# Kernel optimization log

Measured on AMD Instinct MI355X. Metric: run time of the kernel, lower is better.

## Reference

```python
import jax, jax.numpy as jnp
import numpy as np
from jax import lax

EMB, H1, H2 = 100, 128, 64  # embedding_dim, hidden_dim, hidden_dim//2
B, T = 1024, 512


def _uniform(key, shape, scale):
    return jax.random.uniform(key, shape, jnp.float32, -scale, scale)


def setup_inputs() -> dict:
    key = jax.random.key(0)
    ks = jax.random.split(key, 16)
    s1 = 1.0 / np.sqrt(H1)
    s2 = 1.0 / np.sqrt(H2)
    return {
        "X": jax.random.normal(ks[0], (B, T, EMB), jnp.float32),
        # PyTorch LSTM weights, gate order (i, f, g, o)
        "W1_ih": _uniform(ks[1], (4 * H1, EMB), s1),
        "W1_hh": _uniform(ks[2], (4 * H1, H1), s1),
        "b1_ih": _uniform(ks[3], (4 * H1,), s1),
        "b1_hh": _uniform(ks[4], (4 * H1,), s1),
        "W2_ih": _uniform(ks[5], (4 * H2, H1), s2),
        "W2_hh": _uniform(ks[6], (4 * H2, H2), s2),
        "b2_ih": _uniform(ks[7], (4 * H2,), s2),
        "b2_hh": _uniform(ks[8], (4 * H2,), s2),
        "fc1_w": _uniform(ks[9], (32, H2), 1.0 / np.sqrt(H2)),
        "fc1_b": _uniform(ks[10], (32,), 1.0 / np.sqrt(H2)),
        "fc2_w": _uniform(ks[11], (1, 32), 1.0 / np.sqrt(32)),
        "fc2_b": _uniform(ks[12], (1,), 1.0 / np.sqrt(32)),
    }


def _lstm(x, W_ih, W_hh, b_ih, b_hh):
    # x: [B, T, D]; returns (all hidden states [B, T, H], final h [B, H])
    Bb = x.shape[0]
    H = W_hh.shape[1]
    # Batch the input projection across all timesteps (one big GEMM).
    xw = jnp.einsum('btd,gd->tbg', x, W_ih) + (b_ih + b_hh)  # [T, B, 4H]

    def step(carry, xt):
        h, c = carry
        gates = xt + h @ W_hh.T  # [B, 4H]
        i, f, g, o = jnp.split(gates, 4, axis=-1)
        c = jax.nn.sigmoid(f) * c + jax.nn.sigmoid(i) * jnp.tanh(g)
        h = jax.nn.sigmoid(o) * jnp.tanh(c)
        return (h, c), h

    h0 = jnp.zeros((Bb, H), x.dtype)
    (h_n, _), hs = lax.scan(step, (h0, h0), xw)
    return jnp.swapaxes(hs, 0, 1), h_n


def reference(X, W1_ih, W1_hh, b1_ih, b1_hh,
              W2_ih, W2_hh, b2_ih, b2_hh,
              fc1_w, fc1_b, fc2_w, fc2_b):
    hs1, _ = _lstm(X, W1_ih, W1_hh, b1_ih, b1_hh)        # [B, T, 128]
    # dropout is identity at inference
    _, h_n = _lstm(hs1, W2_ih, W2_hh, b2_ih, b2_hh)      # [B, 64]
    x = jax.nn.relu(h_n @ fc1_w.T + fc1_b)               # [B, 32]
    x = x @ fc2_w.T + fc2_b                              # [B, 1]
    return jax.nn.sigmoid(x)[:, 0]                       # [B]
```

## Files before the change

### kernel.cpp

```cpp
#include <hip/hip_runtime.h>
#include <hip/hip_fp16.h>

typedef _Float16 half8 __attribute__((ext_vector_type(8)));
typedef _Float16 half4 __attribute__((ext_vector_type(4)));
typedef float floatx4 __attribute__((ext_vector_type(4)));

#define TT 512
#define EE 100
#define NBATCH 16
#define NBLK 64
#define WS_NEED ((size_t)NBLK * TT * 2048 * sizeof(_Float16))

typedef const __attribute__((address_space(1))) void gvoid_t;
typedef __attribute__((address_space(3))) void lvoid_t;

#define MFMA16 __builtin_amdgcn_mfma_f32_16x16x32_f16

__device__ __forceinline__ float sigm(float x) {
    return __builtin_amdgcn_rcpf(1.0f + __expf(-x));
}
__device__ __forceinline__ float tanh_(float x) {
    return __builtin_amdgcn_rcpf(1.0f + __expf(-2.0f * x)) * 2.0f - 1.0f;
}
__device__ __forceinline__ half4 cvt4(float4 v) {
    half4 h; h[0] = (_Float16)v.x; h[1] = (_Float16)v.y; h[2] = (_Float16)v.z; h[3] = (_Float16)v.w;
    return h;
}

extern "C" __global__ void __launch_bounds__(256)
xfrag_prep(const float* __restrict__ X, _Float16* __restrict__ xw)
{
    const int g   = blockIdx.x >> 5;
    const int t0  = (blockIdx.x & 31) << 4;
    const int tid = threadIdx.x;

    __shared__ __align__(16) _Float16 tile[16][16][120];

    for (int mm = 0; mm < 16; ++mm) {
        const float4* src = (const float4*)(X + ((size_t)(g * 16 + mm) * TT + t0) * EE);
#pragma unroll
        for (int r = 0; r < 2; ++r) {
            const int idx = tid + r * 256;
            if (idx < 400) {
                float4 v = src[idx];
                const int tt = idx / 25, kk = idx - 25 * tt;
                *(half4*)&tile[tt][mm][4 * kk] = cvt4(v);
            }
        }
    }
    __syncthreads();

    const int c = tid >> 4, mm = tid & 15;
    for (int tt = 0; tt < 16; ++tt) {
        half8 v;
        if (c < 12) {
            v = *(const half8*)&tile[tt][mm][8 * c];
        } else if (c == 12) {
            half4 lo = *(const half4*)&tile[tt][mm][96];
            v[0] = lo[0]; v[1] = lo[1]; v[2] = lo[2]; v[3] = lo[3];
            v[4] = (_Float16)1.0f;
            v[5] = (_Float16)0.0f; v[6] = (_Float16)0.0f; v[7] = (_Float16)0.0f;
        } else {
#pragma unroll
            for (int j = 0; j < 8; ++j) v[j] = (_Float16)0.0f;
        }
        *(half8*)&xw[((size_t)(g * TT) + t0 + tt) * 2048 + c * 128 + mm * 8] = v;
    }
}

template<int USE_WS>
__global__ void __launch_bounds__(512, 1)
lstm_regc(const float* __restrict__ X, const _Float16* __restrict__ xw,
          const float* __restrict__ W1ih, const float* __restrict__ W1hh,
          const float* __restrict__ b1i,  const float* __restrict__ b1h,
          const float* __restrict__ W2ih, const float* __restrict__ W2hh,
          const float* __restrict__ b2i,  const float* __restrict__ b2h,
          const float* __restrict__ fc1w, const float* __restrict__ fc1b,
          const float* __restrict__ fc2w, const float* __restrict__ fc2b,
          float* __restrict__ out)
{
    const int tid  = threadIdx.x;
    const int w    = tid >> 6;
    const int lane = tid & 63;
    const int q    = lane >> 4;
    const int m    = lane & 15;
    const int b0   = blockIdx.x * NBATCH;

    __shared__ __align__(16) _Float16 h1b[2 * 2048];
    __shared__ __align__(16) _Float16 h2b[2 * 1024];
    __shared__ __align__(16) _Float16 xb [2 * 2048];
    __shared__ float fca[NBATCH][32];

    for (int i = tid; i < 2 * 1024; i += 512) h2b[i] = (_Float16)0.0f;
    if (!USE_WS) {
        for (int i = tid; i < 2 * 2048; i += 512) {
            const int k = i & 2047;
            xb[i] = (k >= 1536 && k < 1664 && (k & 7) == 4) ? (_Float16)1.0f
                                                            : (_Float16)0.0f;
        }
    }

    half8 w1ihf[4][4], w1hhf[4][4], w2ihf[2][4], w2hhf[2][2];
    floatx4 bias2v[2];
#pragma unroll
    for (int g = 0; g < 4; ++g) {
        const int r = g * 128 + 16 * w + m;
        const float bias = b1i[r] + b1h[r];
#pragma unroll
        for (int s = 0; s < 4; ++s) {
            half8 f;
#pragma unroll
            for (int j = 0; j < 8; ++j) {
                const int k = 32 * s + 8 * q + j;
                float v = 0.0f;
                if (k < EE) v = W1ih[r * EE + k];
                else if (k == EE) v = bias;
                f[j] = (_Float16)v;
            }
            w1ihf[g][s] = f;
        }
#pragma unroll
        for (int s = 0; s < 4; ++s) {
            half8 f;
#pragma unroll
            for (int j = 0; j < 8; ++j) f[j] = (_Float16)W1hh[r * 128 + 32 * s + 8 * q + j];
            w1hhf[g][s] = f;
        }
    }
#pragma unroll
    for (int tau = 0; tau < 2; ++tau) {
        const int rr = (m & 3) * 64 + 8 * w + 4 * tau + (m >> 2);
#pragma unroll
        for (int s = 0; s < 4; ++s) {
            half8 f;
#pragma unroll
            for (int j = 0; j < 8; ++j) f[j] = (_Float16)W2ih[rr * 128 + 32 * s + 8 * q + j];
            w2ihf[tau][s] = f;
        }
#pragma unroll
        for (int s = 0; s < 2; ++s) {
            half8 f;
#pragma unroll
            for (int j = 0; j < 8; ++j) f[j] = (_Float16)W2hh[rr * 64 + 32 * s + 8 * q + j];
            w2hhf[tau][s] = f;
        }
        const int uu = 8 * w + 4 * tau + q;
#pragma unroll
        for (int reg = 0; reg < 4; ++reg)
            bias2v[tau][reg] = b2i[reg * 64 + uu] + b2h[reg * 64 + uu];
    }

    const int foff  = q * 128 + m * 8;
    const int vv    = 2 * w + (q >> 1);
    const int jj    = 4 * (q & 1);
    const int woff1 = (vv >> 2) * 512 + (vv & 3) * 128 + m * 8 + jj;
    int uoff[2];
#pragma unroll
    for (int tau = 0; tau < 2; ++tau) {
        const int u = 8 * w + 4 * tau + q;
        uoff[tau] = (u >> 5) * 512 + ((u >> 3) & 3) * 128 + m * 8 + (u & 7);
    }

    const _Float16* xwb = xw + (size_t)blockIdx.x * TT * 2048;

    int gaddr = 0, laddr = 0;
    bool xval = false;
    float4 xr = {0.f, 0.f, 0.f, 0.f};
    if (!USE_WS) {
        xval = tid < 400;
        const int f = xval ? tid : 0;
        const int n = f / 25, pp = f - 25 * n, e0 = 4 * pp;
        gaddr = (b0 + n) * (TT * EE) + e0;
        const int s = e0 >> 5, qr = (e0 >> 3) & 3, j0 = e0 & 7;
        laddr = ((s * 4 + qr) * 16 + n) * 8 + j0;
    }

    __syncthreads();

    if (USE_WS) {
        if (w < 4) {
            __builtin_amdgcn_global_load_lds((gvoid_t*)(xwb + 0 * 2048 + w * 512 + lane * 8),
                                             (lvoid_t*)(xb + 0 * 2048 + w * 512), 16, 0, 0);
            __builtin_amdgcn_global_load_lds((gvoid_t*)(xwb + 1 * 2048 + w * 512 + lane * 8),
                                             (lvoid_t*)(xb + 1 * 2048 + w * 512), 16, 0, 0);
        }
    } else if (xval) {
        *(half4*)&xb[0 * 2048 + laddr] = cvt4(*(const float4*)&X[gaddr + 0 * EE]);
        *(half4*)&xb[1 * 2048 + laddr] = cvt4(*(const float4*)&X[gaddr + 1 * EE]);
        xr = *(const float4*)&X[gaddr + 2 * EE];
    }
    __syncthreads();

    half8 bx[4], bh[4];
#pragma unroll
    for (int s = 0; s < 4; ++s) {
        bx[s] = *(const half8*)(xb + 0 * 2048 + s * 512 + foff);
#pragma unroll
        for (int j = 0; j < 8; ++j) bh[s][j] = (_Float16)0.0f;
    }

    floatx4 c1 = {0.f, 0.f, 0.f, 0.f};
    float c2[2] = {0.f, 0.f};

#pragma unroll 1
    for (int t = 0; t < TT; ++t) {
        const int cur = t & 1, nxt = cur ^ 1;

        {
            floatx4 a[4];
#pragma unroll
            for (int g = 0; g < 4; ++g) a[g] = (floatx4){0.f, 0.f, 0.f, 0.f};
#pragma unroll
            for (int s = 0; s < 4; ++s) {
#pragma unroll
                for (int g = 0; g < 4; ++g) a[g] = MFMA16(w1ihf[g][s], bx[s], a[g], 0, 0, 0);
            }
#pragma unroll
            for (int s = 0; s < 4; ++s) {
#pragma unroll
                for (int g = 0; g < 4; ++g) a[g] = MFMA16(w1hhf[g][s], bh[s], a[g], 0, 0, 0);
            }
            half4 hv;
#pragma unroll
            for (int r = 0; r < 4; ++r) {
                const float iv = sigm(a[0][r]);
                const float fv = sigm(a[1][r]);
                const float gv = tanh_(a[2][r]);
                const float ov = sigm(a[3][r]);
                const float c  = fv * c1[r] + iv * gv;
                c1[r] = c;
                hv[r] = (_Float16)(ov * tanh_(c));
            }
            *(half4*)&h1b[cur * 2048 + woff1] = hv;
        }
        __syncthreads();

        if (USE_WS) {
            if (w < 4) {
                const int tn = (t + 2 < TT) ? (t + 2) : (TT - 1);
                __builtin_amdgcn_global_load_lds((gvoid_t*)(xwb + (size_t)tn * 2048 + w * 512 + lane * 8),
                                                 (lvoid_t*)(xb + cur * 2048 + w * 512), 16, 0, 0);
            }
        } else if (xval) {
            *(half4*)&xb[cur * 2048 + laddr] = cvt4(xr);
            const int tn = (t + 3 < TT) ? (t + 3) : (TT - 1);
            xr = *(const float4*)&X[gaddr + tn * EE];
        }

        half8 h2f[2];
#pragma unroll
        for (int s = 0; s < 4; ++s) bh[s] = *(const half8*)(h1b + cur * 2048 + s * 512 + foff);
#pragma unroll
        for (int s = 0; s < 2; ++s) h2f[s] = *(const half8*)(h2b + nxt * 1024 + s * 512 + foff);
#pragma unroll
        for (int s = 0; s < 4; ++s) bx[s] = *(const half8*)(xb + nxt * 2048 + s * 512 + foff);

        floatx4 a2[2] = { bias2v[0], bias2v[1] };
#pragma unroll
        for (int s = 0; s < 4; ++s) {
            a2[0] = MFMA16(w2ihf[0][s], bh[s], a2[0], 0, 0, 0);
            a2[1] = MFMA16(w2ihf[1][s], bh[s], a2[1], 0, 0, 0);
        }
#pragma unroll
        for (int s = 0; s < 2; ++s) {
            a2[0] = MFMA16(w2hhf[0][s], h2f[s], a2[0], 0, 0, 0);
            a2[1] = MFMA16(w2hhf[1][s], h2f[s], a2[1], 0, 0, 0);
        }

#pragma unroll
        for (int tau = 0; tau < 2; ++tau) {
            const float iv = sigm(a2[tau][0]);
            const float fv = sigm(a2[tau][1]);
            const float gv = tanh_(a2[tau][2]);
            const float ov = sigm(a2[tau][3]);
            const float c  = fv * c2[tau] + iv * gv;
            c2[tau] = c;
            h2b[cur * 1024 + uoff[tau]] = (_Float16)(ov * tanh_(c));
        }
    }
    __syncthreads();

    {
        const int nb = tid >> 5, o = tid & 31;
        const _Float16* h2p = h2b + 1024 + nb * 8;
        float s = fc1b[o];
#pragma unroll
        for (int k = 0; k < 64; ++k)
            s += fc1w[o * 64 + k] * (float)h2p[(k >> 5) * 512 + ((k >> 3) & 3) * 128 + (k & 7)];
        fca[nb][o] = fmaxf(s, 0.0f);
    }
    __syncthreads();
    if (tid < NBATCH) {
        float s = fc2b[0];
#pragma unroll
        for (int k = 0; k < 32; ++k) s += fc2w[k] * fca[tid][k];
        out[b0 + tid] = sigm(s);
    }
}

extern "C" void kernel_launch(void* const* d_in, const int* in_sizes, int n_in,
                              void* d_out, int out_size, void* d_ws, size_t ws_size,
                              hipStream_t stream) {
    const float* X    = (const float*)d_in[0];
    const float* W1ih = (const float*)d_in[1];
    const float* W1hh = (const float*)d_in[2];
    const float* b1i  = (const float*)d_in[3];
    const float* b1h  = (const float*)d_in[4];
    const float* W2ih = (const float*)d_in[5];
    const float* W2hh = (const float*)d_in[6];
    const float* b2i  = (const float*)d_in[7];
    const float* b2h  = (const float*)d_in[8];
    const float* fc1w = (const float*)d_in[9];
    const float* fc1b = (const float*)d_in[10];
    const float* fc2w = (const float*)d_in[11];
    const float* fc2b = (const float*)d_in[12];
    _Float16* xw = (_Float16*)d_ws;

    if (ws_size >= WS_NEED) {
        hipLaunchKernelGGL(xfrag_prep, dim3(2048), dim3(256), 0, stream, X, xw);
        hipLaunchKernelGGL(lstm_regc<1>, dim3(NBLK), dim3(512), 0, stream,
                           X, xw, W1ih, W1hh, b1i, b1h, W2ih, W2hh, b2i, b2h,
                           fc1w, fc1b, fc2w, fc2b, (float*)d_out);
    } else {
        hipLaunchKernelGGL(lstm_regc<0>, dim3(NBLK), dim3(512), 0, stream,
                           X, xw, W1ih, W1hh, b1i, b1h, W2ih, W2hh, b2i, b2h,
                           fc1w, fc1b, fc2w, fc2b, (float*)d_out);
    }
}
```

Baseline: 1.129 ms.

## Fuse X conversion, software-pipeline the two LSTM layers in one barrier per step

Drops the separate X-to-fp16 prep kernel and workspace path. X is now loaded and converted inside the recurrent kernel through a triple-buffered LDS ring. The loop is restructured so layer 2 for step t-1 and layer 1 for step t run in the same iteration with a single barrier, interleaving their MFMAs and activations, plus a tail step for the last layer-2 update. Gate weights and biases are pre-scaled by -log2(e) or -2log2(e), so sigmoid and tanh use a raw exp2 plus rcp; this adds a little fp16 rounding of the scaled weights.

```diff
diff --git a/kernel.cpp b/kernel.cpp
--- a/kernel.cpp
+++ b/kernel.cpp
@@ -9,75 +9,31 @@
 #define EE 100
 #define NBATCH 16
 #define NBLK 64
-#define WS_NEED ((size_t)NBLK * TT * 2048 * sizeof(_Float16))
-
-typedef const __attribute__((address_space(1))) void gvoid_t;
-typedef __attribute__((address_space(3))) void lvoid_t;
 
 #define MFMA16 __builtin_amdgcn_mfma_f32_16x16x32_f16
-
-__device__ __forceinline__ float sigm(float x) {
-    return __builtin_amdgcn_rcpf(1.0f + __expf(-x));
-}
-__device__ __forceinline__ float tanh_(float x) {
-    return __builtin_amdgcn_rcpf(1.0f + __expf(-2.0f * x)) * 2.0f - 1.0f;
+#define EXP2   __builtin_amdgcn_exp2f
+#define RCP    __builtin_amdgcn_rcpf
+
+#define S_SIG  (-1.44269504088896340736f)
+#define S_TANH (-2.88539008177792681472f)
+
+__device__ __forceinline__ float sigm_slow(float x) {
+    return RCP(1.0f + __expf(-x));
 }
 __device__ __forceinline__ half4 cvt4(float4 v) {
     half4 h; h[0] = (_Float16)v.x; h[1] = (_Float16)v.y; h[2] = (_Float16)v.z; h[3] = (_Float16)v.w;
     return h;
 }
 
-extern "C" __global__ void __launch_bounds__(256)
-xfrag_prep(const float* __restrict__ X, _Float16* __restrict__ xw)
-{
-    const int g   = blockIdx.x >> 5;
-    const int t0  = (blockIdx.x & 31) << 4;
-    const int tid = threadIdx.x;
-
-    __shared__ __align__(16) _Float16 tile[16][16][120];
-
-    for (int mm = 0; mm < 16; ++mm) {
-        const float4* src = (const float4*)(X + ((size_t)(g * 16 + mm) * TT + t0) * EE);
-#pragma unroll
-        for (int r = 0; r < 2; ++r) {
-            const int idx = tid + r * 256;
-            if (idx < 400) {
-                float4 v = src[idx];
-                const int tt = idx / 25, kk = idx - 25 * tt;
-                *(half4*)&tile[tt][mm][4 * kk] = cvt4(v);
-            }
-        }
-    }
-    __syncthreads();
-
-    const int c = tid >> 4, mm = tid & 15;
-    for (int tt = 0; tt < 16; ++tt) {
-        half8 v;
-        if (c < 12) {
-            v = *(const half8*)&tile[tt][mm][8 * c];
-        } else if (c == 12) {
-            half4 lo = *(const half4*)&tile[tt][mm][96];
-            v[0] = lo[0]; v[1] = lo[1]; v[2] = lo[2]; v[3] = lo[3];
-            v[4] = (_Float16)1.0f;
-            v[5] = (_Float16)0.0f; v[6] = (_Float16)0.0f; v[7] = (_Float16)0.0f;
-        } else {
-#pragma unroll
-            for (int j = 0; j < 8; ++j) v[j] = (_Float16)0.0f;
-        }
-        *(half8*)&xw[((size_t)(g * TT) + t0 + tt) * 2048 + c * 128 + mm * 8] = v;
-    }
-}
-
-template<int USE_WS>
 __global__ void __launch_bounds__(512, 1)
-lstm_regc(const float* __restrict__ X, const _Float16* __restrict__ xw,
-          const float* __restrict__ W1ih, const float* __restrict__ W1hh,
-          const float* __restrict__ b1i,  const float* __restrict__ b1h,
-          const float* __restrict__ W2ih, const float* __restrict__ W2hh,
-          const float* __restrict__ b2i,  const float* __restrict__ b2h,
-          const float* __restrict__ fc1w, const float* __restrict__ fc1b,
-          const float* __restrict__ fc2w, const float* __restrict__ fc2b,
-          float* __restrict__ out)
+lstm_fused(const float* __restrict__ X,
+           const float* __restrict__ W1ih, const float* __restrict__ W1hh,
+           const float* __restrict__ b1i,  const float* __restrict__ b1h,
+           const float* __restrict__ W2ih, const float* __restrict__ W2hh,
+           const float* __restrict__ b2i,  const float* __restrict__ b2h,
+           const float* __restrict__ fc1w, const float* __restrict__ fc1b,
+           const float* __restrict__ fc2w, const float* __restrict__ fc2b,
+           float* __restrict__ out)
 {
     const int tid  = threadIdx.x;
     const int w    = tid >> 6;
@@ -88,24 +44,24 @@
 
     __shared__ __align__(16) _Float16 h1b[2 * 2048];
     __shared__ __align__(16) _Float16 h2b[2 * 1024];
-    __shared__ __align__(16) _Float16 xb [2 * 2048];
+    __shared__ __align__(16) _Float16 xb [3 * 2048];
     __shared__ float fca[NBATCH][32];
 
-    for (int i = tid; i < 2 * 1024; i += 512) h2b[i] = (_Float16)0.0f;
-    if (!USE_WS) {
-        for (int i = tid; i < 2 * 2048; i += 512) {
-            const int k = i & 2047;
-            xb[i] = (k >= 1536 && k < 1664 && (k & 7) == 4) ? (_Float16)1.0f
-                                                            : (_Float16)0.0f;
-        }
-    }
+    for (int i = tid; i < 3 * 2048; i += 512) {
+        const int k = i & 2047;
+        xb[i] = (k >= 1536 && k < 1664 && (k & 7) == 4) ? (_Float16)1.0f
+                                                        : (_Float16)0.0f;
+    }
+    for (int i = tid; i < 2048; i += 512) h1b[2048 + i] = (_Float16)0.0f;
+    for (int i = tid; i < 1024; i += 512) h2b[i] = (_Float16)0.0f;
 
     half8 w1ihf[4][4], w1hhf[4][4], w2ihf[2][4], w2hhf[2][2];
     floatx4 bias2v[2];
 #pragma unroll
     for (int g = 0; g < 4; ++g) {
+        const float sg = (g == 2) ? S_TANH : S_SIG;
         const int r = g * 128 + 16 * w + m;
-        const float bias = b1i[r] + b1h[r];
+        const float bias = (b1i[r] + b1h[r]) * sg;
 #pragma unroll
         for (int s = 0; s < 4; ++s) {
             half8 f;
@@ -113,7 +69,7 @@
             for (int j = 0; j < 8; ++j) {
                 const int k = 32 * s + 8 * q + j;
                 float v = 0.0f;
-                if (k < EE) v = W1ih[r * EE + k];
+                if (k < EE) v = W1ih[r * EE + k] * sg;
                 else if (k == EE) v = bias;
                 f[j] = (_Float16)v;
             }
@@ -123,31 +79,36 @@
         for (int s = 0; s < 4; ++s) {
             half8 f;
 #pragma unroll
-            for (int j = 0; j < 8; ++j) f[j] = (_Float16)W1hh[r * 128 + 32 * s + 8 * q + j];
+            for (int j = 0; j < 8; ++j)
+                f[j] = (_Float16)(W1hh[r * 128 + 32 * s + 8 * q + j] * sg);
             w1hhf[g][s] = f;
         }
     }
 #pragma unroll
     for (int tau = 0; tau < 2; ++tau) {
+        const float srow = ((m & 3) == 2) ? S_TANH : S_SIG;
         const int rr = (m & 3) * 64 + 8 * w + 4 * tau + (m >> 2);
 #pragma unroll
         for (int s = 0; s < 4; ++s) {
             half8 f;
 #pragma unroll
-            for (int j = 0; j < 8; ++j) f[j] = (_Float16)W2ih[rr * 128 + 32 * s + 8 * q + j];
+            for (int j = 0; j < 8; ++j)
+                f[j] = (_Float16)(W2ih[rr * 128 + 32 * s + 8 * q + j] * srow);
             w2ihf[tau][s] = f;
         }
 #pragma unroll
         for (int s = 0; s < 2; ++s) {
             half8 f;
 #pragma unroll
-            for (int j = 0; j < 8; ++j) f[j] = (_Float16)W2hh[rr * 64 + 32 * s + 8 * q + j];
+            for (int j = 0; j < 8; ++j)
+                f[j] = (_Float16)(W2hh[rr * 64 + 32 * s + 8 * q + j] * srow);
             w2hhf[tau][s] = f;
         }
         const int uu = 8 * w + 4 * tau + q;
 #pragma unroll
         for (int reg = 0; reg < 4; ++reg)
-            bias2v[tau][reg] = b2i[reg * 64 + uu] + b2h[reg * 64 + uu];
+            bias2v[tau][reg] = (b2i[reg * 64 + uu] + b2h[reg * 64 + uu])
+                               * ((reg == 2) ? S_TANH : S_SIG);
     }
 
     const int foff  = q * 128 + m * 8;
@@ -161,101 +122,48 @@
         uoff[tau] = (u >> 5) * 512 + ((u >> 3) & 3) * 128 + m * 8 + (u & 7);
     }
 
-    const _Float16* xwb = xw + (size_t)blockIdx.x * TT * 2048;
-
-    int gaddr = 0, laddr = 0;
-    bool xval = false;
+    const bool xval = tid < 400;
+    const int f    = xval ? tid : 0;
+    const int n    = f / 25, pp = f - 25 * n, e0 = 4 * pp;
+    const int gaddr = (b0 + n) * (TT * EE) + e0;
+    const int ls = e0 >> 5, lq = (e0 >> 3) & 3, lj = e0 & 7;
+    const int laddr = ls * 512 + lq * 128 + n * 8 + lj;
+
     float4 xr = {0.f, 0.f, 0.f, 0.f};
-    if (!USE_WS) {
-        xval = tid < 400;
-        const int f = xval ? tid : 0;
-        const int n = f / 25, pp = f - 25 * n, e0 = 4 * pp;
-        gaddr = (b0 + n) * (TT * EE) + e0;
-        const int s = e0 >> 5, qr = (e0 >> 3) & 3, j0 = e0 & 7;
-        laddr = ((s * 4 + qr) * 16 + n) * 8 + j0;
-    }
-
-    __syncthreads();
-
-    if (USE_WS) {
-        if (w < 4) {
-            __builtin_amdgcn_global_load_lds((gvoid_t*)(xwb + 0 * 2048 + w * 512 + lane * 8),
-                                             (lvoid_t*)(xb + 0 * 2048 + w * 512), 16, 0, 0);
-            __builtin_amdgcn_global_load_lds((gvoid_t*)(xwb + 1 * 2048 + w * 512 + lane * 8),
-                                             (lvoid_t*)(xb + 1 * 2048 + w * 512), 16, 0, 0);
-        }
-    } else if (xval) {
+    const float* xp = X + gaddr + 3 * EE;
+    if (xval) {
         *(half4*)&xb[0 * 2048 + laddr] = cvt4(*(const float4*)&X[gaddr + 0 * EE]);
         *(half4*)&xb[1 * 2048 + laddr] = cvt4(*(const float4*)&X[gaddr + 1 * EE]);
         xr = *(const float4*)&X[gaddr + 2 * EE];
     }
-    __syncthreads();
-
-    half8 bx[4], bh[4];
-#pragma unroll
-    for (int s = 0; s < 4; ++s) {
-        bx[s] = *(const half8*)(xb + 0 * 2048 + s * 512 + foff);
-#pragma unroll
-        for (int j = 0; j < 8; ++j) bh[s][j] = (_Float16)0.0f;
-    }
 
     floatx4 c1 = {0.f, 0.f, 0.f, 0.f};
     float c2[2] = {0.f, 0.f};
+    int s0 = 0, s1 = 1, s2 = 2;
 
 #pragma unroll 1
     for (int t = 0; t < TT; ++t) {
         const int cur = t & 1, nxt = cur ^ 1;
 
-        {
-            floatx4 a[4];
-#pragma unroll
-            for (int g = 0; g < 4; ++g) a[g] = (floatx4){0.f, 0.f, 0.f, 0.f};
-#pragma unroll
-            for (int s = 0; s < 4; ++s) {
-#pragma unroll
-                for (int g = 0; g < 4; ++g) a[g] = MFMA16(w1ihf[g][s], bx[s], a[g], 0, 0, 0);
-            }
-#pragma unroll
-            for (int s = 0; s < 4; ++s) {
-#pragma unroll
-                for (int g = 0; g < 4; ++g) a[g] = MFMA16(w1hhf[g][s], bh[s], a[g], 0, 0, 0);
-            }
-            half4 hv;
-#pragma unroll
-            for (int r = 0; r < 4; ++r) {
-                const float iv = sigm(a[0][r]);
-                const float fv = sigm(a[1][r]);
-                const float gv = tanh_(a[2][r]);
-                const float ov = sigm(a[3][r]);
-                const float c  = fv * c1[r] + iv * gv;
-                c1[r] = c;
-                hv[r] = (_Float16)(ov * tanh_(c));
-            }
-            *(half4*)&h1b[cur * 2048 + woff1] = hv;
-        }
         __syncthreads();
 
-        if (USE_WS) {
-            if (w < 4) {
-                const int tn = (t + 2 < TT) ? (t + 2) : (TT - 1);
-                __builtin_amdgcn_global_load_lds((gvoid_t*)(xwb + (size_t)tn * 2048 + w * 512 + lane * 8),
-                                                 (lvoid_t*)(xb + cur * 2048 + w * 512), 16, 0, 0);
-            }
-        } else if (xval) {
-            *(half4*)&xb[cur * 2048 + laddr] = cvt4(xr);
-            const int tn = (t + 3 < TT) ? (t + 3) : (TT - 1);
-            xr = *(const float4*)&X[gaddr + tn * EE];
-        }
-
-        half8 h2f[2];
-#pragma unroll
-        for (int s = 0; s < 4; ++s) bh[s] = *(const half8*)(h1b + cur * 2048 + s * 512 + foff);
-#pragma unroll
-        for (int s = 0; s < 2; ++s) h2f[s] = *(const half8*)(h2b + nxt * 1024 + s * 512 + foff);
-#pragma unroll
-        for (int s = 0; s < 4; ++s) bx[s] = *(const half8*)(xb + nxt * 2048 + s * 512 + foff);
-
-        floatx4 a2[2] = { bias2v[0], bias2v[1] };
+        half8 bh[4], bx[4], h2f[2];
+#pragma unroll
+        for (int s = 0; s < 4; ++s) bh[s] = *(const half8*)(h1b + nxt * 2048 + s * 512 + foff);
+#pragma unroll
+        for (int s = 0; s < 2; ++s) h2f[s] = *(const half8*)(h2b + cur * 1024 + s * 512 + foff);
+#pragma unroll
+        for (int s = 0; s < 4; ++s) bx[s] = *(const half8*)(xb + s0 * 2048 + s * 512 + foff);
+
+        if (xval) {
+            *(half4*)&xb[s2 * 2048 + laddr] = cvt4(xr);
+            xr = *(const float4*)xp;
+            if (t < TT - 4) xp += EE;
+        }
+
+        floatx4 a2[2];
+        if (t == 0) { a2[0] = (floatx4){0.f,0.f,0.f,0.f}; a2[1] = (floatx4){0.f,0.f,0.f,0.f}; }
+        else        { a2[0] = bias2v[0]; a2[1] = bias2v[1]; }
 #pragma unroll
         for (int s = 0; s < 4; ++s) {
             a2[0] = MFMA16(w2ihf[0][s], bh[s], a2[0], 0, 0, 0);
@@ -267,15 +175,80 @@
             a2[1] = MFMA16(w2hhf[1][s], h2f[s], a2[1], 0, 0, 0);
         }
 
+        floatx4 a[4];
+#pragma unroll
+        for (int g = 0; g < 4; ++g) a[g] = (floatx4){0.f, 0.f, 0.f, 0.f};
+#pragma unroll
+        for (int s = 0; s < 4; ++s) {
+#pragma unroll
+            for (int g = 0; g < 4; ++g) a[g] = MFMA16(w1ihf[g][s], bx[s], a[g], 0, 0, 0);
+        }
+
 #pragma unroll
         for (int tau = 0; tau < 2; ++tau) {
-            const float iv = sigm(a2[tau][0]);
-            const float fv = sigm(a2[tau][1]);
-            const float gv = tanh_(a2[tau][2]);
-            const float ov = sigm(a2[tau][3]);
+            const float iv = RCP(1.0f + EXP2(a2[tau][0]));
+            const float fv = RCP(1.0f + EXP2(a2[tau][1]));
+            const float gv = fmaf(2.0f, RCP(1.0f + EXP2(a2[tau][2])), -1.0f);
+            const float ov = RCP(1.0f + EXP2(a2[tau][3]));
             const float c  = fv * c2[tau] + iv * gv;
             c2[tau] = c;
-            h2b[cur * 1024 + uoff[tau]] = (_Float16)(ov * tanh_(c));
+            const float th = fmaf(2.0f, RCP(1.0f + EXP2(c * S_TANH)), -1.0f);
+            h2b[nxt * 1024 + uoff[tau]] = (_Float16)(ov * th);
+        }
+
+#pragma unroll
+        for (int s = 0; s < 4; ++s) {
+#pragma unroll
+            for (int g = 0; g < 4; ++g) a[g] = MFMA16(w1hhf[g][s], bh[s], a[g], 0, 0, 0);
+        }
+
+        {
+            half4 hv;
+#pragma unroll
+            for (int r = 0; r < 4; ++r) {
+                const float iv = RCP(1.0f + EXP2(a[0][r]));
+                const float fv = RCP(1.0f + EXP2(a[1][r]));
+                const float gv = fmaf(2.0f, RCP(1.0f + EXP2(a[2][r])), -1.0f);
+                const float ov = RCP(1.0f + EXP2(a[3][r]));
+                const float c  = fv * c1[r] + iv * gv;
+                c1[r] = c;
+                const float th = fmaf(2.0f, RCP(1.0f + EXP2(c * S_TANH)), -1.0f);
+                hv[r] = (_Float16)(ov * th);
+            }
+            *(half4*)&h1b[cur * 2048 + woff1] = hv;
+        }
+
+        const int st = s0; s0 = s1; s1 = s2; s2 = st;
+    }
+
+    __syncthreads();
+    {
+        half8 bh[4], h2f[2];
+#pragma unroll
+        for (int s = 0; s < 4; ++s) bh[s] = *(const half8*)(h1b + 1 * 2048 + s * 512 + foff);
+#pragma unroll
+        for (int s = 0; s < 2; ++s) h2f[s] = *(const half8*)(h2b + 0 * 1024 + s * 512 + foff);
+        floatx4 a2[2] = { bias2v[0], bias2v[1] };
+#pragma unroll
+        for (int s = 0; s < 4; ++s) {
+            a2[0] = MFMA16(w2ihf[0][s], bh[s], a2[0], 0, 0, 0);
+            a2[1] = MFMA16(w2ihf[1][s], bh[s], a2[1], 0, 0, 0);
+        }
+#pragma unroll
+        for (int s = 0; s < 2; ++s) {
+            a2[0] = MFMA16(w2hhf[0][s], h2f[s], a2[0], 0, 0, 0);
+            a2[1] = MFMA16(w2hhf[1][s], h2f[s], a2[1], 0, 0, 0);
+        }
+#pragma unroll
+        for (int tau = 0; tau < 2; ++tau) {
+            const float iv = RCP(1.0f + EXP2(a2[tau][0]));
+            const float fv = RCP(1.0f + EXP2(a2[tau][1]));
+            const float gv = fmaf(2.0f, RCP(1.0f + EXP2(a2[tau][2])), -1.0f);
+            const float ov = RCP(1.0f + EXP2(a2[tau][3]));
+            const float c  = fv * c2[tau] + iv * gv;
+            c2[tau] = c;
+            const float th = fmaf(2.0f, RCP(1.0f + EXP2(c * S_TANH)), -1.0f);
+            h2b[1 * 1024 + uoff[tau]] = (_Float16)(ov * th);
         }
     }
     __syncthreads();
@@ -294,7 +267,7 @@
         float s = fc2b[0];
 #pragma unroll
         for (int k = 0; k < 32; ++k) s += fc2w[k] * fca[tid][k];
-        out[b0 + tid] = sigm(s);
+        out[b0 + tid] = sigm_slow(s);
     }
 }
 
@@ -314,16 +287,8 @@
     const float* fc1b = (const float*)d_in[10];
     const float* fc2w = (const float*)d_in[11];
     const float* fc2b = (const float*)d_in[12];
-    _Float16* xw = (_Float16*)d_ws;
-
-    if (ws_size >= WS_NEED) {
-        hipLaunchKernelGGL(xfrag_prep, dim3(2048), dim3(256), 0, stream, X, xw);
-        hipLaunchKernelGGL(lstm_regc<1>, dim3(NBLK), dim3(512), 0, stream,
-                           X, xw, W1ih, W1hh, b1i, b1h, W2ih, W2hh, b2i, b2h,
-                           fc1w, fc1b, fc2w, fc2b, (float*)d_out);
-    } else {
-        hipLaunchKernelGGL(lstm_regc<0>, dim3(NBLK), dim3(512), 0, stream,
-                           X, xw, W1ih, W1hh, b1i, b1h, W2ih, W2hh, b2i, b2h,
-                           fc1w, fc1b, fc2w, fc2b, (float*)d_out);
-    }
-}
+
+    hipLaunchKernelGGL(lstm_fused, dim3(NBLK), dim3(512), 0, stream,
+                       X, W1ih, W1hh, b1i, b1h, W2ih, W2hh, b2i, b2h,
+                       fc1w, fc1b, fc2w, fc2b, (float*)d_out);
+}
```

After: 948.7 us. 16.0% less time.
